# Performance work log

Measured on AMD Instinct MI355X. Metric: run time of the kernel, lower is better.

Reference implementation:

```python
import jax, jax.numpy as jnp
import numpy as np

B, S, T, E, H = 2, 2048, 2048, 1024, 16
HD = E // H  # head_dim = 64


def setup_inputs() -> dict:
    key = jax.random.key(0)
    ks = jax.random.split(key, 12)
    sc = 1.0 / np.sqrt(E)
    inp = {
        "query": jax.random.normal(ks[0], (B, S, E), jnp.float32),
        "key": jax.random.normal(ks[1], (B, T, E), jnp.float32),
        "value": jax.random.normal(ks[2], (B, T, E), jnp.float32),
        "attn_mask": jnp.ones((S, T), jnp.int32),
        # nn.Linear params: y = x @ W.T + b
        "Wq": jax.random.normal(ks[3], (E, E), jnp.float32) * sc,
        "bq": jax.random.normal(ks[4], (E,), jnp.float32) * sc,
        "Wk": jax.random.normal(ks[5], (E, E), jnp.float32) * sc,
        "bk": jax.random.normal(ks[6], (E,), jnp.float32) * sc,
        "Wv": jax.random.normal(ks[7], (E, E), jnp.float32) * sc,
        "bv": jax.random.normal(ks[8], (E,), jnp.float32) * sc,
        "Wo": jax.random.normal(ks[9], (E, E), jnp.float32) * sc,
        "bo": jax.random.normal(ks[10], (E,), jnp.float32) * sc,
    }
    return inp


def reference(query, key, value, attn_mask, Wq, bq, Wk, bk, Wv, bv, Wo, bo):
    N, Sq, Ed = query.shape
    Tk = key.shape[1]
    # projections (torch Linear: x @ W.T + b)
    q = query @ Wq.T + bq
    k = key @ Wk.T + bk
    v = value @ Wv.T + bv
    # split heads -> (N, H, S, HD)
    q = q.reshape(N, Sq, H, HD).transpose(0, 2, 1, 3)
    k = k.reshape(N, Tk, H, HD).transpose(0, 2, 1, 3)
    v = v.reshape(N, Tk, H, HD).transpose(0, 2, 1, 3)
    # scaled dot-product scores: (N, H, S, T)
    energy = jnp.einsum("nhsd,nhtd->nhst", q, k) / jnp.sqrt(jnp.float32(HD))
    energy = jnp.where(attn_mask[None, None, :, :] == 0, -jnp.inf, energy)
    attn = jax.nn.softmax(energy, axis=3)
    # dropout is identity in eval mode
    out = jnp.einsum("nhst,nhtd->nshd", attn, v).reshape(N, Sq, Ed)
    return out @ Wo.T + bo
```

## Files before the change

### kernel.cpp

```cpp
#include <hip/hip_runtime.h>

typedef __attribute__((ext_vector_type(8))) short short8;
typedef __attribute__((ext_vector_type(4))) float f32x4;
typedef __attribute__((ext_vector_type(16))) float f32x16;

#define DEV __device__ __forceinline__

constexpr int Bb = 2, Ss = 2048, Tt = 2048, Ee = 1024, Hh = 16, HDd = 64;
constexpr int Mm = Bb * Ss;
constexpr size_t NX = (size_t)Mm * Ee;
constexpr size_t NW = (size_t)Ee * Ee;

constexpr size_t OFF_XQ   = 0;
constexpr size_t OFF_XK   = OFF_XQ + NX * 2;
constexpr size_t OFF_XV   = OFF_XK + NX * 2;
constexpr size_t OFF_WQ   = OFF_XV + NX * 2;
constexpr size_t OFF_WK   = OFF_WQ + NW * 2;
constexpr size_t OFF_WV   = OFF_WK + NW * 2;
constexpr size_t OFF_WO   = OFF_WV + NW * 2;
constexpr size_t OFF_QH   = OFF_WO + NW * 2;
constexpr size_t OFF_KH   = OFF_QH + NX * 2;
constexpr size_t OFF_VH   = OFF_KH + NX * 2;
constexpr size_t OFF_OB   = OFF_VH + NX * 2;
constexpr size_t OFF_FLAG = OFF_OB + NX * 2;

DEV unsigned short f2bf(float f) {
  union { float f; unsigned u; } v; v.f = f;
  unsigned r = v.u + 0x7fffu + ((v.u >> 16) & 1u);
  return (unsigned short)(r >> 16);
}

#define GLDS16(g, l) __builtin_amdgcn_global_load_lds(                         \
    (const __attribute__((address_space(1))) void*)(g),                        \
    (__attribute__((address_space(3))) void*)(l), 16, 0, 0)

#define PLSWAP(a, b) asm("v_permlane32_swap_b32 %0, %1" : "+v"(a), "+v"(b))
#define CVTPK(d, lo, hi_) asm("v_cvt_pk_bf16_f32 %0, %1, %2" : "=v"(d) : "v"(lo), "v"(hi_))

#if __has_builtin(__builtin_amdgcn_exp2f)
#define EXP2(x) __builtin_amdgcn_exp2f(x)
#else
#define EXP2(x) __expf((x) * 0.69314718f)
#endif

constexpr float SCLQ = 0.18033688f;

__global__ __launch_bounds__(256) void prep_kernel(
    const float* __restrict__ wq, const float* __restrict__ wk,
    const float* __restrict__ wv, const float* __restrict__ wo,
    const int* __restrict__ mask,
    unsigned short* __restrict__ Wqb, unsigned short* __restrict__ Wkb,
    unsigned short* __restrict__ Wvb, unsigned short* __restrict__ Wob,
    int* __restrict__ flagZero)
{
  constexpr size_t NWv = NW / 4, NXv = NX / 4;
  constexpr size_t tot = 4 * NWv + NXv;
  for (size_t u = (size_t)blockIdx.x * blockDim.x + threadIdx.x; u < tot;
       u += (size_t)gridDim.x * blockDim.x) {
    if (u < 4 * NWv) {
      int wsel = (int)(u / NWv); size_t off = u % NWv;
      const float* src = wsel == 0 ? wq : wsel == 1 ? wk : wsel == 2 ? wv : wo;
      unsigned short* dst = wsel == 0 ? Wqb : wsel == 1 ? Wkb : wsel == 2 ? Wvb : Wob;
      float4 f = ((const float4*)src)[off];
      ushort4 o; o.x = f2bf(f.x); o.y = f2bf(f.y); o.z = f2bf(f.z); o.w = f2bf(f.w);
      ((ushort4*)dst)[off] = o;
    } else {
      size_t off = u - 4 * NWv;
      int4 m = ((const int4*)mask)[off];
      if (m.x == 0 || m.y == 0 || m.z == 0 || m.w == 0) *flagZero = 1;
    }
  }
}

DEV void gemm128_f32A(const float* __restrict__ Af, const unsigned short* __restrict__ Bm,
                      unsigned short (*Asm)[128 * 32], unsigned short (*Bsm)[128 * 32],
                      f32x4 acc[4][4], int K)
{
  const int t = threadIdx.x;
  const int w = t >> 6, lane = t & 63;
  const int l15 = lane & 15, l4 = lane >> 4;
  const int wm = w >> 1, wn = w & 1;
  const int srow = lane >> 2;
  const int skc  = (lane & 3) * 8;
  const int ar = t >> 2;
  const int ak = (t & 3) * 8;
#pragma unroll
  for (int mi = 0; mi < 4; ++mi)
#pragma unroll
    for (int ni = 0; ni < 4; ++ni) acc[mi][ni] = (f32x4){0.f, 0.f, 0.f, 0.f};

  float4 a0, a1, a2, a3;
#define ALOAD(k0)                                                            \
  { const float* ap  = Af + (size_t)ar * K + (k0) + ak;                      \
    const float* ap2 = ap + (size_t)64 * K;                                  \
    a0 = *(const float4*)ap;  a1 = *(const float4*)(ap + 4);                 \
    a2 = *(const float4*)ap2; a3 = *(const float4*)(ap2 + 4); }
#define BSTAGE(d, k0)                                                        \
  { GLDS16(Bm + (size_t)(w * 16 + srow) * K + (k0) + skc,      Bsm[d] + w * 512);        \
    GLDS16(Bm + (size_t)(64 + w * 16 + srow) * K + (k0) + skc, Bsm[d] + 2048 + w * 512); }
#define AWRITE(d)                                                            \
  { unsigned u0, u1, u2, u3, u4, u5, u6, u7;                                 \
    CVTPK(u0, a0.x, a0.y); CVTPK(u1, a0.z, a0.w);                            \
    CVTPK(u2, a1.x, a1.y); CVTPK(u3, a1.z, a1.w);                            \
    CVTPK(u4, a2.x, a2.y); CVTPK(u5, a2.z, a2.w);                            \
    CVTPK(u6, a3.x, a3.y); CVTPK(u7, a3.z, a3.w);                            \
    union { unsigned u[4]; short8 s; } p0, p1;                               \
    p0.u[0] = u0; p0.u[1] = u1; p0.u[2] = u2; p0.u[3] = u3;                  \
    p1.u[0] = u4; p1.u[1] = u5; p1.u[2] = u6; p1.u[3] = u7;                  \
    *(short8*)&Asm[d][ar * 32 + ak]        = p0.s;                           \
    *(short8*)&Asm[d][(64 + ar) * 32 + ak] = p1.s; }

  ALOAD(0) BSTAGE(0, 0)
  asm volatile("s_waitcnt vmcnt(0)" ::: "memory");
  AWRITE(0)
  __syncthreads();

  int it = 0;
  for (int k0 = 0; k0 < K; k0 += 32, ++it) {
    const int cur = it & 1;
    const bool more = (k0 + 32 < K);
    if (more) { ALOAD(k0 + 32) BSTAGE(cur ^ 1, k0 + 32) }

    short8 af[4], bf[4];
#pragma unroll
    for (int mi = 0; mi < 4; ++mi)
      af[mi] = *(const short8*)&Asm[cur][(wm * 64 + mi * 16 + l15) * 32 + l4 * 8];
#pragma unroll
    for (int ni = 0; ni < 4; ++ni)
      bf[ni] = *(const short8*)&Bsm[cur][(wn * 64 + ni * 16 + l15) * 32 + l4 * 8];
    __builtin_amdgcn_s_setprio(1);
#pragma unroll
    for (int mi = 0; mi < 4; ++mi)
#pragma unroll
      for (int ni = 0; ni < 4; ++ni)
        acc[mi][ni] = __builtin_amdgcn_mfma_f32_16x16x32_bf16(af[mi], bf[ni], acc[mi][ni], 0, 0, 0);
    __builtin_amdgcn_s_setprio(0);

    if (more) {
      asm volatile("s_waitcnt vmcnt(0)" ::: "memory");
      AWRITE(cur ^ 1)
    }
    __syncthreads();
  }
#undef ALOAD
#undef BSTAGE
#undef AWRITE
}

DEV void gemm128_8w(const unsigned short* __restrict__ A, const unsigned short* __restrict__ Bm,
                    unsigned short (*Asm)[128 * 32], unsigned short (*Bsm)[128 * 32],
                    f32x4 acc[2][4], int K)
{
  const int tid = threadIdx.x, w = tid >> 6, lane = tid & 63;
  const int l15 = lane & 15, l4 = lane >> 4;
  const int wm = w >> 1, wn = w & 1;
  const int grow = tid >> 2, gk = (tid & 3) * 8;
#pragma unroll
  for (int mi = 0; mi < 2; ++mi)
#pragma unroll
    for (int ni = 0; ni < 4; ++ni) acc[mi][ni] = (f32x4){0.f, 0.f, 0.f, 0.f};

#define GSTAGE8(d, k0)                                                   \
  {                                                                      \
    GLDS16(A  + (size_t)grow * K + (k0) + gk, Asm[d] + w * 512);         \
    GLDS16(Bm + (size_t)grow * K + (k0) + gk, Bsm[d] + w * 512);         \
  }

  GSTAGE8(0, 0)
  int it = 0;
  for (int k0 = 0; k0 < K; k0 += 32, ++it) {
    const int cur = it & 1;
    asm volatile("s_waitcnt vmcnt(0)" ::: "memory");
    __builtin_amdgcn_s_barrier();
    if (k0 + 32 < K) GSTAGE8(cur ^ 1, k0 + 32)

    short8 af[2], bf[4];
#pragma unroll
    for (int mi = 0; mi < 2; ++mi)
      af[mi] = *(const short8*)&Asm[cur][(wm * 32 + mi * 16 + l15) * 32 + l4 * 8];
#pragma unroll
    for (int ni = 0; ni < 4; ++ni)
      bf[ni] = *(const short8*)&Bsm[cur][(wn * 64 + ni * 16 + l15) * 32 + l4 * 8];
    __builtin_amdgcn_s_setprio(1);
#pragma unroll
    for (int mi = 0; mi < 2; ++mi)
#pragma unroll
      for (int ni = 0; ni < 4; ++ni)
        acc[mi][ni] = __builtin_amdgcn_mfma_f32_16x16x32_bf16(af[mi], bf[ni], acc[mi][ni], 0, 0, 0);
    __builtin_amdgcn_s_setprio(0);
  }
#undef GSTAGE8
}

__global__ __launch_bounds__(256, 3) void gemm_qkv(
    const float* __restrict__ q, const float* __restrict__ k, const float* __restrict__ v,
    const unsigned short* __restrict__ Wqb, const unsigned short* __restrict__ Wkb,
    const unsigned short* __restrict__ Wvb,
    const float* __restrict__ bq, const float* __restrict__ bk, const float* __restrict__ bv,
    unsigned short* __restrict__ Qh, unsigned short* __restrict__ Kh, unsigned short* __restrict__ Vh)
{
  __shared__ unsigned short Asm[2][128 * 32], Bsm[2][128 * 32];
  const int orig = (blockIdx.z * 32 + blockIdx.y) * 8 + blockIdx.x;
  const int sid  = (orig & 7) * 96 + (orig >> 3);
  const int z  = sid >> 8;
  const int by = (sid & 255) >> 3, bx = sid & 7;
  const float* A           = (z == 0) ? q   : (z == 1) ? k   : v;
  const unsigned short* Bw = (z == 0) ? Wqb : (z == 1) ? Wkb : Wvb;
  const float* bias        = (z == 0) ? bq  : (z == 1) ? bk  : bv;
  unsigned short* Out      = (z == 0) ? Qh  : (z == 1) ? Kh  : Vh;
  f32x4 acc[4][4];
  gemm128_f32A(A + (size_t)by * 128 * Ee, Bw + (size_t)bx * 128 * Ee, Asm, Bsm, acc, Ee);
  const int t = threadIdx.x, w = t >> 6, lane = t & 63, l15 = lane & 15, l4 = lane >> 4;
  const int wm = w >> 1, wn = w & 1;
  if (z < 2) {
    const float osc = (z == 0) ? SCLQ : 1.0f;
#pragma unroll
    for (int ni = 0; ni < 4; ++ni) {
      int col = bx * 128 + wn * 64 + ni * 16 + l15;
      float bcol = bias[col];
      int h = col >> 6, hd = col & 63;
#pragma unroll
      for (int mi = 0; mi < 4; ++mi) {
#pragma unroll
        for (int r = 0; r < 4; ++r) {
          int row = by * 128 + wm * 64 + mi * 16 + l4 * 4 + r;
          int b = row >> 11, s = row & 2047;
          Out[(((size_t)(b * Hh + h)) * Ss + s) * HDd + hd] = f2bf((acc[mi][ni][r] + bcol) * osc);
        }
      }
    }
  } else {
#pragma unroll
    for (int ni = 0; ni < 4; ++ni) {
      int col = bx * 128 + wn * 64 + ni * 16 + l15;
      float bcol = bias[col];
      int h = col >> 6, hd = col & 63;
#pragma unroll
      for (int mi = 0; mi < 4; ++mi) {
        int row = by * 128 + wm * 64 + mi * 16 + l4 * 4;
        int b = row >> 11, s = row & 2047;
        ushort4 pk;
        pk.x = f2bf(acc[mi][ni][0] + bcol); pk.y = f2bf(acc[mi][ni][1] + bcol);
        pk.z = f2bf(acc[mi][ni][2] + bcol); pk.w = f2bf(acc[mi][ni][3] + bcol);
        *(ushort4*)&Out[((size_t)((b * Hh + h) * HDd + hd)) * Ss + s] = pk;
      }
    }
  }
}

__global__ __launch_bounds__(512) void gemm_out(
    const unsigned short* __restrict__ Ob, const unsigned short* __restrict__ Wob,
    const float* __restrict__ bo, float* __restrict__ out)
{
  __shared__ unsigned short Asm[2][128 * 32], Bsm[2][128 * 32];
  const int orig = blockIdx.y * 8 + blockIdx.x;
  const int sid  = (orig & 7) * 32 + (orig >> 3);
  const int by = sid >> 3, bx = sid & 7;
  f32x4 acc[2][4];
  gemm128_8w(Ob + (size_t)by * 128 * Ee, Wob + (size_t)bx * 128 * Ee, Asm, Bsm, acc, Ee);
  const int tid = threadIdx.x, w = tid >> 6, lane = tid & 63;
  const int l15 = lane & 15, l4 = lane >> 4;
  const int wm = w >> 1, wn = w & 1;
#pragma unroll
  for (int ni = 0; ni < 4; ++ni) {
    int col = bx * 128 + wn * 64 + ni * 16 + l15;
    float bcol = bo[col];
#pragma unroll
    for (int mi = 0; mi < 2; ++mi) {
#pragma unroll
      for (int r = 0; r < 4; ++r) {
        int row = by * 128 + wm * 32 + mi * 16 + l4 * 4 + r;
        out[(size_t)row * Ee + col] = acc[mi][ni][r] + bcol;
      }
    }
  }
}

__global__ __launch_bounds__(256, 4) void attn_kernel(
    const unsigned short* __restrict__ Qh, const unsigned short* __restrict__ Kh,
    const unsigned short* __restrict__ Vh, const int* __restrict__ mask,
    const int* __restrict__ flagZero, unsigned short* __restrict__ Ob)
{
  __shared__ unsigned short Ks[2][64 * 64];
  __shared__ unsigned short Vs[2][64 * 64];
  const int bh = blockIdx.y, qt = blockIdx.x;
  const int tid = threadIdx.x, w = tid >> 6, lane = tid & 63;
  const int l31 = lane & 31, hi = lane >> 5;
  const int g = w >> 1, p = w & 1;
  const bool useMask = (*flagZero != 0);
  const size_t bhBase = (size_t)bh * Ss * HDd;
  const int s0 = qt * 64 + g * 32;
  const int trow = p * 32 + l31;

  short8 qf[4];
#pragma unroll
  for (int ks = 0; ks < 4; ++ks)
    qf[ks] = *(const short8*)&Qh[bhBase + (size_t)(s0 + l31) * 64 + ks * 16 + hi * 8];

  f32x16 o0, o1, Z16;
#pragma unroll
  for (int r = 0; r < 16; ++r) { o0[r] = 0.f; o1[r] = 0.f; Z16[r] = 0.f; }
  float l_r = 0.f;

  const int cRow = tid >> 3, cG = (tid & 7) ^ (cRow & 7);

#define STAGE(d, kt2)                                                                         \
  {                                                                                           \
    _Pragma("unroll")                                                                         \
    for (int i = 0; i < 2; ++i)                                                               \
      GLDS16(Kh + bhBase + (size_t)((kt2) + i * 32 + cRow) * 64 + cG * 8,                     \
             &Ks[d][0] + (i * 256 + w * 64) * 8);                                             \
    _Pragma("unroll")                                                                         \
    for (int i = 0; i < 2; ++i)                                                               \
      GLDS16(Vh + bhBase + (size_t)(i * 32 + cRow) * Ss + (kt2) + cG * 8,                     \
             &Vs[d][0] + (i * 256 + w * 64) * 8);                                             \
  }

#define SMPACK(kt2)                                                                           \
  {                                                                                           \
    if (useMask) {                                                                            \
      int sg = s0 + l31;                                                                      \
      _Pragma("unroll")                                                                       \
      for (int r = 0; r < 16; ++r) {                                                          \
        int tg = (kt2) + p * 32 + (r & 3) + 8 * (r >> 2) + 4 * hi;                            \
        if (mask[(size_t)sg * Tt + tg] == 0) pr[r] = -1e30f;                                  \
      }                                                                                       \
    }                                                                                         \
    _Pragma("unroll")                                                                         \
    for (int r = 0; r < 16; ++r) pr[r] = EXP2(pr[r]);                                         \
    float a0 = (pr[0] + pr[1]) + (pr[2] + pr[3]);                                             \
    float a1 = (pr[4] + pr[5]) + (pr[6] + pr[7]);                                             \
    float a2 = (pr[8] + pr[9]) + (pr[10] + pr[11]);                                           \
    float a3 = (pr[12] + pr[13]) + (pr[14] + pr[15]);                                         \
    l_r += (a0 + a1) + (a2 + a3);                                                             \
    _Pragma("unroll")                                                                         \
    for (int h2 = 0; h2 < 2; ++h2) {                                                          \
      unsigned c0, c1, d0, d1; const int bse = h2 * 8;                                        \
      CVTPK(c0, pr[bse + 0], pr[bse + 1]);                                                    \
      CVTPK(c1, pr[bse + 2], pr[bse + 3]);                                                    \
      CVTPK(d0, pr[bse + 4], pr[bse + 5]);                                                    \
      CVTPK(d1, pr[bse + 6], pr[bse + 7]);                                                    \
      PLSWAP(c0, d0); PLSWAP(c1, d1);                                                         \
      union { unsigned u[4]; short8 s; } cc;                                                  \
      cc.u[0] = c0; cc.u[1] = c1; cc.u[2] = d0; cc.u[3] = d1;                                 \
      pa[h2] = cc.s;                                                                          \
    }                                                                                         \
  }

  f32x16 pr;
  short8 pa[2];

  STAGE(0, 0)
  asm volatile("s_waitcnt vmcnt(2)" ::: "memory");
  __builtin_amdgcn_s_barrier();
  STAGE(1, 64)
  {
    const unsigned short* Kc = &Ks[0][0];
    short8 ka = *(const short8*)&Kc[trow * 64 + ((hi ^ (l31 & 7)) * 8)];
    pr = __builtin_amdgcn_mfma_f32_32x32x16_bf16(ka, qf[0], Z16, 0, 0, 0);
#pragma unroll
    for (int ks = 1; ks < 4; ++ks) {
      short8 kb = *(const short8*)&Kc[trow * 64 + (((ks * 2 + hi) ^ (l31 & 7)) * 8)];
      pr = __builtin_amdgcn_mfma_f32_32x32x16_bf16(kb, qf[ks], pr, 0, 0, 0);
    }
  }
  SMPACK(0)

  for (int t = 0; t < 32; ++t) {
    const int cur = t & 1;
    if (t < 31) { asm volatile("s_waitcnt vmcnt(2)" ::: "memory"); }
    else        { asm volatile("s_waitcnt vmcnt(0)" ::: "memory"); }
    __builtin_amdgcn_s_barrier();

    const unsigned short* Vc = &Vs[cur][0];
    __builtin_amdgcn_s_setprio(1);
    if (t < 31) {
      const unsigned short* Kn = &Ks[cur ^ 1][0];
      short8 ka0 = *(const short8*)&Kn[trow * 64 + (((0 + hi) ^ (l31 & 7)) * 8)];
      short8 ka1 = *(const short8*)&Kn[trow * 64 + (((2 + hi) ^ (l31 & 7)) * 8)];
      short8 ka2 = *(const short8*)&Kn[trow * 64 + (((4 + hi) ^ (l31 & 7)) * 8)];
      short8 ka3 = *(const short8*)&Kn[trow * 64 + (((6 + hi) ^ (l31 & 7)) * 8)];
      short8 vf00 = *(const short8*)&Vc[l31 * 64 + (((p * 4 + 0 + hi) ^ (l31 & 7)) * 8)];
      short8 vf01 = *(const short8*)&Vc[(32 + l31) * 64 + (((p * 4 + 0 + hi) ^ ((l31 & 7))) * 8)];
      short8 vf10 = *(const short8*)&Vc[l31 * 64 + (((p * 4 + 2 + hi) ^ (l31 & 7)) * 8)];
      short8 vf11 = *(const short8*)&Vc[(32 + l31) * 64 + (((p * 4 + 2 + hi) ^ ((l31 & 7))) * 8)];
      f32x16 prN;
      prN = __builtin_amdgcn_mfma_f32_32x32x16_bf16(ka0, qf[0], Z16, 0, 0, 0);
      o0  = __builtin_amdgcn_mfma_f32_32x32x16_bf16(pa[0], vf00, o0, 0, 0, 0);
      o1  = __builtin_amdgcn_mfma_f32_32x32x16_bf16(pa[0], vf01, o1, 0, 0, 0);
      prN = __builtin_amdgcn_mfma_f32_32x32x16_bf16(ka1, qf[1], prN, 0, 0, 0);
      o0  = __builtin_amdgcn_mfma_f32_32x32x16_bf16(pa[1], vf10, o0, 0, 0, 0);
      prN = __builtin_amdgcn_mfma_f32_32x32x16_bf16(ka2, qf[2], prN, 0, 0, 0);
      o1  = __builtin_amdgcn_mfma_f32_32x32x16_bf16(pa[1], vf11, o1, 0, 0, 0);
      prN = __builtin_amdgcn_mfma_f32_32x32x16_bf16(ka3, qf[3], prN, 0, 0, 0);
      pr = prN;
    } else {
      short8 vf00 = *(const short8*)&Vc[l31 * 64 + (((p * 4 + 0 + hi) ^ (l31 & 7)) * 8)];
      short8 vf01 = *(const short8*)&Vc[(32 + l31) * 64 + (((p * 4 + 0 + hi) ^ ((l31 & 7))) * 8)];
      short8 vf10 = *(const short8*)&Vc[l31 * 64 + (((p * 4 + 2 + hi) ^ (l31 & 7)) * 8)];
      short8 vf11 = *(const short8*)&Vc[(32 + l31) * 64 + (((p * 4 + 2 + hi) ^ ((l31 & 7))) * 8)];
      o0 = __builtin_amdgcn_mfma_f32_32x32x16_bf16(pa[0], vf00, o0, 0, 0, 0);
      o1 = __builtin_amdgcn_mfma_f32_32x32x16_bf16(pa[0], vf01, o1, 0, 0, 0);
      o0 = __builtin_amdgcn_mfma_f32_32x32x16_bf16(pa[1], vf10, o0, 0, 0, 0);
      o1 = __builtin_amdgcn_mfma_f32_32x32x16_bf16(pa[1], vf11, o1, 0, 0, 0);
    }
    __builtin_amdgcn_s_setprio(0);

    if (t < 31) SMPACK((t + 1) * 64)

    __builtin_amdgcn_s_barrier();
    if (t < 30) STAGE(cur, (t + 2) * 64)
  }
#undef STAGE
#undef SMPACK

  __syncthreads();

  float* Ox = (float*)&Ks[0][0];
  float* Ml = (float*)&Vs[0][0];
  float lt = l_r + __shfl_xor(l_r, 32);
  if (p == 1) {
#pragma unroll
    for (int r = 0; r < 16; ++r) {
      int sr = (r & 3) + 8 * (r >> 2) + 4 * hi;
      Ox[g * 2048 + sr * 64 + l31]      = o0[r];
      Ox[g * 2048 + sr * 64 + 32 + l31] = o1[r];
    }
    if (hi == 0) Ml[g * 32 + l31] = lt;
  }
  __syncthreads();
  if (p == 0) {
    const int b = bh >> 4, h = bh & 15;
    float ltot = lt + Ml[g * 32 + l31];
    float linv = ltot > 0.f ? 1.0f / ltot : 0.f;
#pragma unroll
    for (int r = 0; r < 16; ++r) {
      int sr = (r & 3) + 8 * (r >> 2) + 4 * hi;
      float li = __shfl(linv, sr);
      size_t rowbase = (size_t)(b * Ss + s0 + sr) * Ee + h * 64;
      Ob[rowbase + l31]      = f2bf((o0[r] + Ox[g * 2048 + sr * 64 + l31]) * li);
      Ob[rowbase + 32 + l31] = f2bf((o1[r] + Ox[g * 2048 + sr * 64 + 32 + l31]) * li);
    }
  }
}

extern "C" void kernel_launch(void* const* d_in, const int* in_sizes, int n_in,
                              void* d_out, int out_size, void* d_ws, size_t ws_size,
                              hipStream_t stream) {
  const float* q   = (const float*)d_in[0];
  const float* k   = (const float*)d_in[1];
  const float* v   = (const float*)d_in[2];
  const int*  msk  = (const int*)d_in[3];
  const float* Wq  = (const float*)d_in[4];
  const float* bq  = (const float*)d_in[5];
  const float* Wk  = (const float*)d_in[6];
  const float* bk  = (const float*)d_in[7];
  const float* Wv  = (const float*)d_in[8];
  const float* bv  = (const float*)d_in[9];
  const float* Wo  = (const float*)d_in[10];
  const float* bo  = (const float*)d_in[11];
  float* out = (float*)d_out;

  char* ws = (char*)d_ws;
  unsigned short* Wqb = (unsigned short*)(ws + OFF_WQ);
  unsigned short* Wkb = (unsigned short*)(ws + OFF_WK);
  unsigned short* Wvb = (unsigned short*)(ws + OFF_WV);
  unsigned short* Wob = (unsigned short*)(ws + OFF_WO);
  unsigned short* Qh  = (unsigned short*)(ws + OFF_QH);
  unsigned short* Kh  = (unsigned short*)(ws + OFF_KH);
  unsigned short* Vh  = (unsigned short*)(ws + OFF_VH);
  unsigned short* Ob  = (unsigned short*)(ws + OFF_OB);
  int* flagZero       = (int*)(ws + OFF_FLAG);

  hipMemsetAsync(flagZero, 0, 4, stream);
  prep_kernel<<<2048, 256, 0, stream>>>(Wq, Wk, Wv, Wo, msk,
                                        Wqb, Wkb, Wvb, Wob, flagZero);
  gemm_qkv<<<dim3(8, 32, 3), 256, 0, stream>>>(q, k, v, Wqb, Wkb, Wvb,
                                               bq, bk, bv, Qh, Kh, Vh);
  attn_kernel<<<dim3(32, 32), 256, 0, stream>>>(Qh, Kh, Vh, msk, flagZero, Ob);
  gemm_out<<<dim3(8, 32), 512, 0, stream>>>(Ob, Wob, bo, out);
}
```

Before: 122.0 us.

## Deepen fp32-A prefetch pipeline in QKV GEMM with fine-grained vmcnt waits

The QKV projection GEMM loop is restructured so the fp32 A operand is prefetched two K-steps ahead using two register sets. Full vmcnt(0) waits are replaced with partial vmcnt/lgkmcnt waits and raw s_barrier, so global loads overlap the MFMA compute instead of draining each iteration. The loop is manually unrolled by two with a peeled epilogue, and launch bounds are raised to 4 blocks per CU. The extra register buffers together with the higher occupancy target may force spills or lower achieved occupancy, and the counter-based waits depend on exact load ordering. Unused offsets for the bf16 input staging buffers are also removed.

```diff
diff --git a/kernel.cpp b/kernel.cpp
--- a/kernel.cpp
+++ b/kernel.cpp
@@ -11,10 +11,7 @@
 constexpr size_t NX = (size_t)Mm * Ee;
 constexpr size_t NW = (size_t)Ee * Ee;
 
-constexpr size_t OFF_XQ   = 0;
-constexpr size_t OFF_XK   = OFF_XQ + NX * 2;
-constexpr size_t OFF_XV   = OFF_XK + NX * 2;
-constexpr size_t OFF_WQ   = OFF_XV + NX * 2;
+constexpr size_t OFF_WQ   = 0;
 constexpr size_t OFF_WK   = OFF_WQ + NW * 2;
 constexpr size_t OFF_WV   = OFF_WK + NW * 2;
 constexpr size_t OFF_WO   = OFF_WV + NW * 2;
@@ -89,62 +86,82 @@
 #pragma unroll
     for (int ni = 0; ni < 4; ++ni) acc[mi][ni] = (f32x4){0.f, 0.f, 0.f, 0.f};
 
-  float4 a0, a1, a2, a3;
-#define ALOAD(k0)                                                            \
+  float4 x0, x1, x2, x3;
+  float4 y0, y1, y2, y3;
+
+#define ALOAD(r0, r1, r2, r3, k0)                                            \
   { const float* ap  = Af + (size_t)ar * K + (k0) + ak;                      \
     const float* ap2 = ap + (size_t)64 * K;                                  \
-    a0 = *(const float4*)ap;  a1 = *(const float4*)(ap + 4);                 \
-    a2 = *(const float4*)ap2; a3 = *(const float4*)(ap2 + 4); }
+    r0 = *(const float4*)ap;  r1 = *(const float4*)(ap + 4);                 \
+    r2 = *(const float4*)ap2; r3 = *(const float4*)(ap2 + 4); }
 #define BSTAGE(d, k0)                                                        \
   { GLDS16(Bm + (size_t)(w * 16 + srow) * K + (k0) + skc,      Bsm[d] + w * 512);        \
     GLDS16(Bm + (size_t)(64 + w * 16 + srow) * K + (k0) + skc, Bsm[d] + 2048 + w * 512); }
-#define AWRITE(d)                                                            \
+#define AWRITE(d, r0, r1, r2, r3)                                            \
   { unsigned u0, u1, u2, u3, u4, u5, u6, u7;                                 \
-    CVTPK(u0, a0.x, a0.y); CVTPK(u1, a0.z, a0.w);                            \
-    CVTPK(u2, a1.x, a1.y); CVTPK(u3, a1.z, a1.w);                            \
-    CVTPK(u4, a2.x, a2.y); CVTPK(u5, a2.z, a2.w);                            \
-    CVTPK(u6, a3.x, a3.y); CVTPK(u7, a3.z, a3.w);                            \
+    CVTPK(u0, r0.x, r0.y); CVTPK(u1, r0.z, r0.w);                            \
+    CVTPK(u2, r1.x, r1.y); CVTPK(u3, r1.z, r1.w);                            \
+    CVTPK(u4, r2.x, r2.y); CVTPK(u5, r2.z, r2.w);                            \
+    CVTPK(u6, r3.x, r3.y); CVTPK(u7, r3.z, r3.w);                            \
     union { unsigned u[4]; short8 s; } p0, p1;                               \
     p0.u[0] = u0; p0.u[1] = u1; p0.u[2] = u2; p0.u[3] = u3;                  \
     p1.u[0] = u4; p1.u[1] = u5; p1.u[2] = u6; p1.u[3] = u7;                  \
     *(short8*)&Asm[d][ar * 32 + ak]        = p0.s;                           \
     *(short8*)&Asm[d][(64 + ar) * 32 + ak] = p1.s; }
-
-  ALOAD(0) BSTAGE(0, 0)
+#define COMP(cur)                                                            \
+  { short8 af[4], bf[4];                                                     \
+    _Pragma("unroll")                                                        \
+    for (int mi = 0; mi < 4; ++mi)                                           \
+      af[mi] = *(const short8*)&Asm[cur][(wm * 64 + mi * 16 + l15) * 32 + l4 * 8]; \
+    _Pragma("unroll")                                                        \
+    for (int ni = 0; ni < 4; ++ni)                                           \
+      bf[ni] = *(const short8*)&Bsm[cur][(wn * 64 + ni * 16 + l15) * 32 + l4 * 8]; \
+    __builtin_amdgcn_s_setprio(1);                                           \
+    _Pragma("unroll")                                                        \
+    for (int mi = 0; mi < 4; ++mi)                                           \
+      _Pragma("unroll")                                                      \
+      for (int ni = 0; ni < 4; ++ni)                                         \
+        acc[mi][ni] = __builtin_amdgcn_mfma_f32_16x16x32_bf16(af[mi], bf[ni], acc[mi][ni], 0, 0, 0); \
+    __builtin_amdgcn_s_setprio(0); }
+
+  ALOAD(x0, x1, x2, x3, 0)
+  BSTAGE(0, 0)
+  asm volatile("s_waitcnt vmcnt(2)" ::: "memory");
+  AWRITE(0, x0, x1, x2, x3)
+  ALOAD(y0, y1, y2, y3, 32)
+  asm volatile("s_waitcnt vmcnt(4)" ::: "memory");
+  asm volatile("s_waitcnt lgkmcnt(0)" ::: "memory");
+  __builtin_amdgcn_s_barrier();
+
+  const int nt = K / 32;
+  for (int tt = 0; tt + 2 < nt; tt += 2) {
+    BSTAGE(1, (tt + 1) * 32)
+    ALOAD(x0, x1, x2, x3, (tt + 2) * 32)
+    COMP(0)
+    asm volatile("s_waitcnt vmcnt(4)" ::: "memory");
+    AWRITE(1, y0, y1, y2, y3)
+    asm volatile("s_waitcnt lgkmcnt(0)" ::: "memory");
+    __builtin_amdgcn_s_barrier();
+    BSTAGE(0, (tt + 2) * 32)
+    ALOAD(y0, y1, y2, y3, (tt + 3) * 32)
+    COMP(1)
+    asm volatile("s_waitcnt vmcnt(4)" ::: "memory");
+    AWRITE(0, x0, x1, x2, x3)
+    asm volatile("s_waitcnt lgkmcnt(0)" ::: "memory");
+    __builtin_amdgcn_s_barrier();
+  }
+  BSTAGE(1, (nt - 1) * 32)
+  COMP(0)
+  asm volatile("s_waitcnt vmcnt(2)" ::: "memory");
+  AWRITE(1, y0, y1, y2, y3)
+  asm volatile("s_waitcnt lgkmcnt(0)" ::: "memory");
+  __builtin_amdgcn_s_barrier();
   asm volatile("s_waitcnt vmcnt(0)" ::: "memory");
-  AWRITE(0)
-  __syncthreads();
-
-  int it = 0;
-  for (int k0 = 0; k0 < K; k0 += 32, ++it) {
-    const int cur = it & 1;
-    const bool more = (k0 + 32 < K);
-    if (more) { ALOAD(k0 + 32) BSTAGE(cur ^ 1, k0 + 32) }
-
-    short8 af[4], bf[4];
-#pragma unroll
-    for (int mi = 0; mi < 4; ++mi)
-      af[mi] = *(const short8*)&Asm[cur][(wm * 64 + mi * 16 + l15) * 32 + l4 * 8];
-#pragma unroll
-    for (int ni = 0; ni < 4; ++ni)
-      bf[ni] = *(const short8*)&Bsm[cur][(wn * 64 + ni * 16 + l15) * 32 + l4 * 8];
-    __builtin_amdgcn_s_setprio(1);
-#pragma unroll
-    for (int mi = 0; mi < 4; ++mi)
-#pragma unroll
-      for (int ni = 0; ni < 4; ++ni)
-        acc[mi][ni] = __builtin_amdgcn_mfma_f32_16x16x32_bf16(af[mi], bf[ni], acc[mi][ni], 0, 0, 0);
-    __builtin_amdgcn_s_setprio(0);
-
-    if (more) {
-      asm volatile("s_waitcnt vmcnt(0)" ::: "memory");
-      AWRITE(cur ^ 1)
-    }
-    __syncthreads();
-  }
+  COMP(1)
 #undef ALOAD
 #undef BSTAGE
 #undef AWRITE
+#undef COMP
 }
 
 DEV void gemm128_8w(const unsigned short* __restrict__ A, const unsigned short* __restrict__ Bm,
@@ -192,7 +209,7 @@
 #undef GSTAGE8
 }
 
-__global__ __launch_bounds__(256, 3) void gemm_qkv(
+__global__ __launch_bounds__(256, 4) void gemm_qkv(
     const float* __restrict__ q, const float* __restrict__ k, const float* __restrict__ v,
     const unsigned short* __restrict__ Wqb, const unsigned short* __restrict__ Wkb,
     const unsigned short* __restrict__ Wvb,
```

After: 166.3 us. +36.4%, slower.
